# Performance work log

Measured on AMD Instinct MI355X. Metric: run time of the kernel, lower is better.

## Reference

```python
import jax, jax.numpy as jnp
import numpy as np

B, S, E, H, SN, LMAX = 128, 512, 768, 16, 100, 5
DH = E // H  # 48

def setup_inputs() -> dict:
    key = jax.random.key(0)
    ks = jax.random.split(key, 10)
    idx = jax.random.randint(ks[0], (B, LMAX), 0, S)
    lengths = jax.random.randint(ks[1], (B,), 1, LMAX + 1)
    valid = jnp.arange(LMAX)[None, :] < lengths[:, None]
    locations = jnp.where(valid, idx, -1)
    return {
        "last_hidden_state": jax.random.normal(ks[2], (B, S, E), jnp.float32),
        "sense_emb": jax.random.normal(ks[3], (B, SN, E), jnp.float32),
        "locations": locations,
        "in_proj_weight": jax.random.normal(ks[4], (3 * E, E), jnp.float32) * 0.02,
        "in_proj_bias": jax.random.normal(ks[5], (3 * E,), jnp.float32) * 0.02,
        "out_proj_weight": jax.random.normal(ks[6], (E, E), jnp.float32) * 0.02,
        "out_proj_bias": jax.random.normal(ks[7], (E,), jnp.float32) * 0.02,
        "linear_weight": jax.random.normal(ks[8], (SN, E), jnp.float32) * 0.02,
        "linear_bias": jax.random.normal(ks[9], (SN,), jnp.float32) * 0.02,
    }

def reference(last_hidden_state, sense_emb, locations, in_proj_weight, in_proj_bias,
              out_proj_weight, out_proj_bias, linear_weight, linear_bias):
    # Ragged gather + mean over the valid (non -1) token locations per row.
    mask = (locations != -1)                                   # [B, LMAX]
    safe = jnp.where(mask, locations, 0)                       # [B, LMAX]
    gathered = jnp.take_along_axis(last_hidden_state, safe[..., None], axis=1)  # [B,LMAX,E]
    cnt = mask.sum(axis=1, keepdims=True).astype(last_hidden_state.dtype)
    pun = (gathered * mask[..., None]).sum(axis=1) / cnt       # [B, E]

    # qkv: prepend pun-word embedding to the sense embeddings -> [B, SN+1, E]
    qkv = jnp.concatenate([pun[:, None, :], sense_emb], axis=1)

    # nn.MultiheadAttention with batch_first=False: axis0 = seq (L=B), axis1 = batch (N=SN+1).
    proj = qkv @ in_proj_weight.T + in_proj_bias               # [L, N, 3E]
    q, k, v = jnp.split(proj, 3, axis=-1)
    L, N = qkv.shape[0], qkv.shape[1]
    q = q.reshape(L, N, H, DH) * (DH ** -0.5)
    k = k.reshape(L, N, H, DH)
    v = v.reshape(L, N, H, DH)
    scores = jnp.einsum('lnhd,mnhd->nhlm', q, k)               # [N,H,L,L]
    attn = jax.nn.softmax(scores, axis=-1)
    ctx = jnp.einsum('nhlm,mnhd->lnhd', attn, v).reshape(L, N, E)
    attn_out = ctx @ out_proj_weight.T + out_proj_bias         # [L, N, E]

    res = attn_out[:, 0, :]                                    # [B, E] (batch slot 0)
    res = res @ linear_weight.T + linear_bias                  # [B, SN]
    return res
```

## Files before the change

kernel.cpp:

```cpp
#include <hip/hip_runtime.h>

#define SEQ 512
#define EMB 768
#define K3E 2304
#define DHD 48

__global__ __launch_bounds__(256) void k1_gemm1(
    const float* __restrict__ lhs, const int* __restrict__ loc,
    const float* __restrict__ Bw, const float* __restrict__ bias,
    float* __restrict__ C)
{
  __shared__ float lds[7168];
  const int t  = threadIdx.x;
  const int w  = t >> 6, l = t & 63;
  const int bm = blockIdx.y * 16, bn = blockIdx.x * 32;
  const int tx = l & 7, ty = l >> 3;
  const int gm = l & 15, gq = l >> 4;
  const int bl = l & 31, bh = l >> 5;
  const int kbase = w * 192;
  const int AW = w * 1792, BW = AW + 640;

  int locs[5]; int cnt = 0;
#pragma unroll
  for (int j = 0; j < 5; j++) {
    int v = loc[(bm + gm) * 5 + j];
    locs[j] = v; if (v >= 0) cnt++;
  }
  const float ginv = 1.0f / (float)cnt;
  const float* lrow = lhs + (size_t)(bm + gm) * SEQ * EMB;
  const float* brow = Bw + (size_t)(bn + bl) * EMB;

  float4 aF, bF0, bF1;

#define K1_LOAD(s) {                                                         \
    int k0 = kbase + (s) * 16;                                               \
    float sx=0.f, sy=0.f, sz=0.f, sw=0.f;                                    \
    _Pragma("unroll")                                                        \
    for (int j = 0; j < 5; j++) {                                            \
      int v = locs[j] >= 0 ? locs[j] : 0;                                    \
      float4 wv = *(const float4*)&lrow[(size_t)v * EMB + k0 + gq * 4];      \
      if (locs[j] >= 0) { sx+=wv.x; sy+=wv.y; sz+=wv.z; sw+=wv.w; }          \
    }                                                                        \
    aF = make_float4(sx*ginv, sy*ginv, sz*ginv, sw*ginv);                    \
    bF0 = *(const float4*)&brow[k0 + bh * 8 + 0];                            \
    bF1 = *(const float4*)&brow[k0 + bh * 8 + 4]; }

#define K1_WRITE(b) {                                                        \
    int Ab = AW + (b) * 320;                                                 \
    lds[Ab + (gq*4+0)*20 + gm] = aF.x;                                       \
    lds[Ab + (gq*4+1)*20 + gm] = aF.y;                                       \
    lds[Ab + (gq*4+2)*20 + gm] = aF.z;                                       \
    lds[Ab + (gq*4+3)*20 + gm] = aF.w;                                       \
    int Bb = BW + (b) * 576;                                                 \
    lds[Bb + (bh*8+0)*36 + bl] = bF0.x; lds[Bb + (bh*8+1)*36 + bl] = bF0.y;  \
    lds[Bb + (bh*8+2)*36 + bl] = bF0.z; lds[Bb + (bh*8+3)*36 + bl] = bF0.w;  \
    lds[Bb + (bh*8+4)*36 + bl] = bF1.x; lds[Bb + (bh*8+5)*36 + bl] = bF1.y;  \
    lds[Bb + (bh*8+6)*36 + bl] = bF1.z; lds[Bb + (bh*8+7)*36 + bl] = bF1.w; }

  float acc[2][4] = {};
  K1_LOAD(0); K1_WRITE(0);
  for (int s = 0; s < 12; s++) {
    int b = s & 1;
    if (s < 11) K1_LOAD(s + 1);
    int Ab = AW + b * 320, Bb = BW + b * 576;
#pragma unroll
    for (int kk = 0; kk < 16; kk++) {
      float2 a  = *(float2*)&lds[Ab + kk * 20 + ty * 2];
      float4 bb = *(float4*)&lds[Bb + kk * 36 + tx * 4];
      acc[0][0] += a.x*bb.x; acc[0][1] += a.x*bb.y; acc[0][2] += a.x*bb.z; acc[0][3] += a.x*bb.w;
      acc[1][0] += a.y*bb.x; acc[1][1] += a.y*bb.y; acc[1][2] += a.y*bb.z; acc[1][3] += a.y*bb.w;
    }
    if (s < 11) K1_WRITE(b ^ 1);
  }
#undef K1_LOAD
#undef K1_WRITE

#pragma unroll
  for (int i = 0; i < 2; i++)
    *(float4*)&lds[AW + (ty*2 + i) * 32 + tx * 4] =
        make_float4(acc[i][0], acc[i][1], acc[i][2], acc[i][3]);
  __syncthreads();
  int o = t * 2;
  int m = o >> 5, n = o & 31;
  float2 s0 = *(float2*)&lds[0*1792 + o];
  float2 s1 = *(float2*)&lds[1*1792 + o];
  float2 s2 = *(float2*)&lds[2*1792 + o];
  float2 s3 = *(float2*)&lds[3*1792 + o];
  float2 bb2 = *(const float2*)&bias[bn + n];
  float2 r = make_float2(s0.x+s1.x+s2.x+s3.x+bb2.x, s0.y+s1.y+s2.y+s3.y+bb2.y);
  *(float2*)&C[(size_t)(bm + m) * K3E + bn + n] = r;
}

__global__ __launch_bounds__(256) void k2_attn_wcomb(
    const float* __restrict__ proj, float* __restrict__ ctx,
    const float* __restrict__ wlin, const float* __restrict__ wout,
    float* __restrict__ wcomb)
{
  __shared__ float lds[13312];
  const int t = threadIdx.x;

  if (blockIdx.x < 128) {
    float* ks = lds;
    float* vs = lds + 6656;
    int h  = blockIdx.x >> 3;
    int l0 = (blockIdx.x & 7) * 16;

    for (int i = t; i < 128 * 12; i += 256) {
      int m  = i / 12;
      int dd = (i - m * 12) * 4;
      float4 kv = *(const float4*)&proj[(size_t)m * K3E + EMB     + h * DHD + dd];
      float4 vv = *(const float4*)&proj[(size_t)m * K3E + 2 * EMB + h * DHD + dd];
      *(float4*)&ks[m * 52 + dd] = kv;
      *(float4*)&vs[m * 52 + dd] = vv;
    }

    int l  = t >> 4;
    int g  = t & 15;
    int lg = l0 + l;
    const float scale = 0.14433756729740643f;
    float q[48];
#pragma unroll
    for (int jj = 0; jj < 12; jj++) {
      float4 qv = *(const float4*)&proj[(size_t)lg * K3E + h * DHD + jj * 4];
      q[jj*4+0] = qv.x * scale; q[jj*4+1] = qv.y * scale;
      q[jj*4+2] = qv.z * scale; q[jj*4+3] = qv.w * scale;
    }
    __syncthreads();

    float sv[8];
    float smax = -1e30f;
#pragma unroll
    for (int jm = 0; jm < 8; jm++) {
      int m = g + jm * 16;
      float s = 0.0f;
#pragma unroll
      for (int dq = 0; dq < 12; dq++) {
        float4 kv = *(const float4*)&ks[m * 52 + dq * 4];
        s += q[dq*4+0]*kv.x + q[dq*4+1]*kv.y + q[dq*4+2]*kv.z + q[dq*4+3]*kv.w;
      }
      sv[jm] = s;
      smax = fmaxf(smax, s);
    }
#pragma unroll
    for (int off = 1; off < 16; off <<= 1) smax = fmaxf(smax, __shfl_xor(smax, off));
    float ssum = 0.0f;
#pragma unroll
    for (int jm = 0; jm < 8; jm++) { float e = __expf(sv[jm] - smax); sv[jm] = e; ssum += e; }
#pragma unroll
    for (int off = 1; off < 16; off <<= 1) ssum += __shfl_xor(ssum, off);
    float inv = 1.0f / ssum;
#pragma unroll
    for (int jm = 0; jm < 8; jm++) sv[jm] *= inv;

    float acc[48] = {};
#pragma unroll
    for (int jm = 0; jm < 8; jm++) {
      int m = g + jm * 16;
      float p = sv[jm];
#pragma unroll
      for (int dq = 0; dq < 12; dq++) {
        float4 vv = *(const float4*)&vs[m * 52 + dq * 4];
        acc[dq*4+0] += p*vv.x; acc[dq*4+1] += p*vv.y;
        acc[dq*4+2] += p*vv.z; acc[dq*4+3] += p*vv.w;
      }
    }

    {
      float buf[24];
      if (g & 8) {
#pragma unroll
        for (int d = 0; d < 24; d++) buf[d] = acc[d];
      } else {
#pragma unroll
        for (int d = 0; d < 24; d++) buf[d] = acc[d + 24];
      }
#pragma unroll
      for (int d = 0; d < 24; d++) buf[d] = __shfl_xor(buf[d], 8);
      if (g & 8) {
#pragma unroll
        for (int d = 0; d < 24; d++) acc[d] = acc[d + 24] + buf[d];
      } else {
#pragma unroll
        for (int d = 0; d < 24; d++) acc[d] = acc[d] + buf[d];
      }
    }
    {
      float buf[12];
      if (g & 4) {
#pragma unroll
        for (int d = 0; d < 12; d++) buf[d] = acc[d];
      } else {
#pragma unroll
        for (int d = 0; d < 12; d++) buf[d] = acc[d + 12];
      }
#pragma unroll
      for (int d = 0; d < 12; d++) buf[d] = __shfl_xor(buf[d], 4);
      if (g & 4) {
#pragma unroll
        for (int d = 0; d < 12; d++) acc[d] = acc[d + 12] + buf[d];
      } else {
#pragma unroll
        for (int d = 0; d < 12; d++) acc[d] = acc[d] + buf[d];
      }
    }
    {
      float buf[6];
      if (g & 2) {
#pragma unroll
        for (int d = 0; d < 6; d++) buf[d] = acc[d];
      } else {
#pragma unroll
        for (int d = 0; d < 6; d++) buf[d] = acc[d + 6];
      }
#pragma unroll
      for (int d = 0; d < 6; d++) buf[d] = __shfl_xor(buf[d], 2);
      if (g & 2) {
#pragma unroll
        for (int d = 0; d < 6; d++) acc[d] = acc[d + 6] + buf[d];
      } else {
#pragma unroll
        for (int d = 0; d < 6; d++) acc[d] = acc[d] + buf[d];
      }
    }
    {
      float buf[3];
      if (g & 1) {
#pragma unroll
        for (int d = 0; d < 3; d++) buf[d] = acc[d];
      } else {
#pragma unroll
        for (int d = 0; d < 3; d++) buf[d] = acc[d + 3];
      }
#pragma unroll
      for (int d = 0; d < 3; d++) buf[d] = __shfl_xor(buf[d], 1);
      if (g & 1) {
#pragma unroll
        for (int d = 0; d < 3; d++) acc[d] = acc[d + 3] + buf[d];
      } else {
#pragma unroll
        for (int d = 0; d < 3; d++) acc[d] = acc[d] + buf[d];
      }
    }
#pragma unroll
    for (int j = 0; j < 3; j++) {
      ctx[(size_t)lg * EMB + h * DHD + g * 3 + j] = acc[j];
    }
  } else {
    const int c  = blockIdx.x - 128;
    const int bm = (c / 24) * 16;
    const int bn = (c % 24) * 32;
    const int w  = t >> 6, l = t & 63;
    const int tx = l & 7, ty = l >> 3;
    const int am = l & 15, aq = l >> 4;
    const int wi = l >> 2;
    const int j4 = (l & 3) * 8;
    const int kbase = w * 192;
    const int AW = w * 1792, BW = AW + 640;

    int arow_i = bm + am; if (arow_i > 99) arow_i = 99;
    const float* arow = wlin + (size_t)arow_i * EMB;

    float4 aF, bF0, bF1;

#define W_LOAD(s) {                                                          \
    int k0 = kbase + (s) * 16;                                               \
    aF  = *(const float4*)&arow[k0 + aq * 4];                                \
    const float* wr = wout + (size_t)(k0 + wi) * EMB + bn + j4;              \
    bF0 = *(const float4*)&wr[0];                                            \
    bF1 = *(const float4*)&wr[4]; }

#define W_WRITE(b) {                                                         \
    int Ab = AW + (b) * 320;                                                 \
    lds[Ab + (aq*4+0)*20 + am] = aF.x;                                       \
    lds[Ab + (aq*4+1)*20 + am] = aF.y;                                       \
    lds[Ab + (aq*4+2)*20 + am] = aF.z;                                       \
    lds[Ab + (aq*4+3)*20 + am] = aF.w;                                       \
    int Bb = BW + (b) * 576;                                                 \
    *(float4*)&lds[Bb + wi*36 + j4]     = bF0;                               \
    *(float4*)&lds[Bb + wi*36 + j4 + 4] = bF1; }

    float acc[2][4] = {};
    W_LOAD(0); W_WRITE(0);
    for (int s = 0; s < 12; s++) {
      int b = s & 1;
      if (s < 11) W_LOAD(s + 1);
      int Ab = AW + b * 320, Bb = BW + b * 576;
#pragma unroll
      for (int kk = 0; kk < 16; kk++) {
        float2 a  = *(float2*)&lds[Ab + kk * 20 + ty * 2];
        float4 bb = *(float4*)&lds[Bb + kk * 36 + tx * 4];
        acc[0][0] += a.x*bb.x; acc[0][1] += a.x*bb.y; acc[0][2] += a.x*bb.z; acc[0][3] += a.x*bb.w;
        acc[1][0] += a.y*bb.x; acc[1][1] += a.y*bb.y; acc[1][2] += a.y*bb.z; acc[1][3] += a.y*bb.w;
      }
      if (s < 11) W_WRITE(b ^ 1);
    }
#undef W_LOAD
#undef W_WRITE

#pragma unroll
    for (int i = 0; i < 2; i++)
      *(float4*)&lds[AW + (ty*2 + i) * 32 + tx * 4] =
          make_float4(acc[i][0], acc[i][1], acc[i][2], acc[i][3]);
    __syncthreads();
    int o = t * 2;
    int m = o >> 5, n = o & 31;
    if (bm + m < 100) {
      float2 s0 = *(float2*)&lds[0*1792 + o];
      float2 s1 = *(float2*)&lds[1*1792 + o];
      float2 s2 = *(float2*)&lds[2*1792 + o];
      float2 s3 = *(float2*)&lds[3*1792 + o];
      float2 r = make_float2(s0.x+s1.x+s2.x+s3.x, s0.y+s1.y+s2.y+s3.y);
      *(float2*)&wcomb[(size_t)(bm + m) * EMB + bn + n] = r;
    }
  }
}

__global__ __launch_bounds__(256) void k3_final(
    const float* __restrict__ A, const float* __restrict__ Bw,
    const float* __restrict__ wlin, const float* __restrict__ bout,
    const float* __restrict__ blin, float* __restrict__ C)
{
  __shared__ float lds[7200];
  const int t  = threadIdx.x;
  const int w  = t >> 6, l = t & 63;
  const int bm = blockIdx.y * 16, bn = blockIdx.x * 32;
  const int tx = l & 7, ty = l >> 3;
  const int am = l & 15, aq = l >> 4;
  const int bl = l & 31, bh = l >> 5;
  const int kbase = w * 192;
  const int AW = w * 1792, BW = AW + 640;

  {
    int col = bn + (t >> 3);
    int ks  = (t & 7) * 96;
    float p = 0.f;
    if (col < 100) {
      const float* wr = wlin + (size_t)col * EMB + ks;
#pragma unroll
      for (int j = 0; j < 24; j++) {
        float4 wv = *(const float4*)&wr[j * 4];
        float4 bv = *(const float4*)&bout[ks + j * 4];
        p += wv.x*bv.x + wv.y*bv.y + wv.z*bv.z + wv.w*bv.w;
      }
    }
    p += __shfl_xor(p, 1); p += __shfl_xor(p, 2); p += __shfl_xor(p, 4);
    if ((t & 7) == 0) lds[7168 + (t >> 3)] = p + (col < 100 ? blin[col] : 0.f);
  }

  const float* arow = A + (size_t)(bm + am) * EMB;
  int brow_i = bn + bl; if (brow_i > 99) brow_i = 99;
  const float* brow = Bw + (size_t)brow_i * EMB;

  float4 aF, bF0, bF1;

#define F_LOAD(s) {                                                          \
    int k0 = kbase + (s) * 16;                                               \
    aF  = *(const float4*)&arow[k0 + aq * 4];                                \
    bF0 = *(const float4*)&brow[k0 + bh * 8 + 0];                            \
    bF1 = *(const float4*)&brow[k0 + bh * 8 + 4]; }

#define F_WRITE(b) {                                                         \
    int Ab = AW + (b) * 320;                                                 \
    lds[Ab + (aq*4+0)*20 + am] = aF.x;                                       \
    lds[Ab + (aq*4+1)*20 + am] = aF.y;                                       \
    lds[Ab + (aq*4+2)*20 + am] = aF.z;                                       \
    lds[Ab + (aq*4+3)*20 + am] = aF.w;                                       \
    int Bb = BW + (b) * 576;                                                 \
    lds[Bb + (bh*8+0)*36 + bl] = bF0.x; lds[Bb + (bh*8+1)*36 + bl] = bF0.y;  \
    lds[Bb + (bh*8+2)*36 + bl] = bF0.z; lds[Bb + (bh*8+3)*36 + bl] = bF0.w;  \
    lds[Bb + (bh*8+4)*36 + bl] = bF1.x; lds[Bb + (bh*8+5)*36 + bl] = bF1.y;  \
    lds[Bb + (bh*8+6)*36 + bl] = bF1.z; lds[Bb + (bh*8+7)*36 + bl] = bF1.w; }

  float acc[2][4] = {};
  F_LOAD(0); F_WRITE(0);
  for (int s = 0; s < 12; s++) {
    int b = s & 1;
    if (s < 11) F_LOAD(s + 1);
    int Ab = AW + b * 320, Bb = BW + b * 576;
#pragma unroll
    for (int kk = 0; kk < 16; kk++) {
      float2 a  = *(float2*)&lds[Ab + kk * 20 + ty * 2];
      float4 bb = *(float4*)&lds[Bb + kk * 36 + tx * 4];
      acc[0][0] += a.x*bb.x; acc[0][1] += a.x*bb.y; acc[0][2] += a.x*bb.z; acc[0][3] += a.x*bb.w;
      acc[1][0] += a.y*bb.x; acc[1][1] += a.y*bb.y; acc[1][2] += a.y*bb.z; acc[1][3] += a.y*bb.w;
    }
    if (s < 11) F_WRITE(b ^ 1);
  }
#undef F_LOAD
#undef F_WRITE

#pragma unroll
  for (int i = 0; i < 2; i++)
    *(float4*)&lds[AW + (ty*2 + i) * 32 + tx * 4] =
        make_float4(acc[i][0], acc[i][1], acc[i][2], acc[i][3]);
  __syncthreads();
  int o = t * 2;
  int m = o >> 5, n = o & 31;
#pragma unroll
  for (int j = 0; j < 2; j++) {
    int col = bn + n + j;
    if (col < 100) {
      float v = lds[0*1792 + o + j] + lds[1*1792 + o + j] +
                lds[2*1792 + o + j] + lds[3*1792 + o + j] + lds[7168 + n + j];
      C[(size_t)(bm + m) * 100 + col] = v;
    }
  }
}

extern "C" void kernel_launch(void* const* d_in, const int* in_sizes, int n_in,
                              void* d_out, int out_size, void* d_ws, size_t ws_size,
                              hipStream_t stream) {
  const float* lhs   = (const float*)d_in[0];
  const int*   loc   = (const int*)  d_in[2];
  const float* w_in  = (const float*)d_in[3];
  const float* b_in  = (const float*)d_in[4];
  const float* w_out = (const float*)d_in[5];
  const float* b_out = (const float*)d_in[6];
  const float* w_lin = (const float*)d_in[7];
  const float* b_lin = (const float*)d_in[8];
  float* out = (float*)d_out;

  char* ws = (char*)d_ws;
  float* proj  = (float*)(ws);
  float* ctx   = (float*)(ws + 1179648);
  float* wcomb = (float*)(ws + 1179648 + 393216);

  k1_gemm1<<<dim3(72, 8), 256, 0, stream>>>(lhs, loc, w_in, b_in, proj);
  k2_attn_wcomb<<<296, 256, 0, stream>>>(proj, ctx, w_lin, w_out, wcomb);
  k3_final<<<dim3(4, 8), 256, 0, stream>>>(ctx, wcomb, w_lin, b_out, b_lin, out);
}
```

Baseline: 51.70 us.

## Split pun gather into own kernel, move wcomb GEMM into first GEMM launch, widen split-K

The ragged gather-mean moves out of the QKV GEMM into a separate small kernel, so the GEMM no longer re-gathers hidden-state rows for every N tile. The Wout·Wlin combination GEMM moves from the attention launch into the QKV GEMM launch, so attention runs alone. The GEMMs now use 512-thread blocks with 8-way split-K instead of 4-way. This shortens the serial K loop and raises parallelism, at the cost of one extra launch, a pun round trip through global memory, and an 8-way LDS reduction.

Result: faster. 45.93 us (-11.2%).

```diff
diff --git a/kernel.cpp b/kernel.cpp
--- a/kernel.cpp
+++ b/kernel.cpp
@@ -5,47 +5,349 @@
 #define K3E 2304
 #define DHD 48
 
-__global__ __launch_bounds__(256) void k1_gemm1(
+__global__ __launch_bounds__(256) void k0_pun(
     const float* __restrict__ lhs, const int* __restrict__ loc,
-    const float* __restrict__ Bw, const float* __restrict__ bias,
-    float* __restrict__ C)
+    float* __restrict__ pun)
 {
-  __shared__ float lds[7168];
-  const int t  = threadIdx.x;
-  const int w  = t >> 6, l = t & 63;
+  int id = blockIdx.x * 256 + threadIdx.x;
+  int row = id / 192;
+  int ch  = id - row * 192;
+  int cnt = 0;
+  float4 s = make_float4(0.f, 0.f, 0.f, 0.f);
+#pragma unroll
+  for (int j = 0; j < 5; j++) {
+    int v = loc[row * 5 + j];
+    if (v >= 0) {
+      float4 wv = *(const float4*)&lhs[((size_t)row * SEQ + v) * EMB + ch * 4];
+      s.x += wv.x; s.y += wv.y; s.z += wv.z; s.w += wv.w;
+      cnt++;
+    }
+  }
+  float inv = 1.0f / (float)cnt;
+  *(float4*)&pun[(size_t)row * EMB + ch * 4] =
+      make_float4(s.x * inv, s.y * inv, s.z * inv, s.w * inv);
+}
+
+__global__ __launch_bounds__(512, 4) void k1_gemm_wcomb(
+    const float* __restrict__ pun, const float* __restrict__ Bw,
+    const float* __restrict__ bias, float* __restrict__ C,
+    const float* __restrict__ wlin, const float* __restrict__ wout,
+    float* __restrict__ wcomb)
+{
+  __shared__ float lds[14336];
+  const int t = threadIdx.x;
+  const int w = t >> 6, l = t & 63;
+  const int tx = l & 7, ty = l >> 3;
+  const int gm = l & 15, gq = l >> 4;
+  const int kbase = w * 96;
+  const int AW = w * 1792, BW = AW + 640;
+
+  float4 aF, bF0, bF1;
+  float acc[2][4] = {};
+
+#define STAGE_A(b) {                                                         \
+    int Ab = AW + (b) * 320;                                                 \
+    lds[Ab + (gq*4+0)*20 + gm] = aF.x;                                       \
+    lds[Ab + (gq*4+1)*20 + gm] = aF.y;                                       \
+    lds[Ab + (gq*4+2)*20 + gm] = aF.z;                                       \
+    lds[Ab + (gq*4+3)*20 + gm] = aF.w; }
+
+#define INNER(b) {                                                           \
+    int Ab = AW + (b) * 320, Bb = BW + (b) * 576;                            \
+    _Pragma("unroll")                                                        \
+    for (int kk = 0; kk < 16; kk++) {                                        \
+      float2 a  = *(float2*)&lds[Ab + kk * 20 + ty * 2];                     \
+      float4 bb = *(float4*)&lds[Bb + kk * 36 + tx * 4];                     \
+      acc[0][0] += a.x*bb.x; acc[0][1] += a.x*bb.y;                          \
+      acc[0][2] += a.x*bb.z; acc[0][3] += a.x*bb.w;                          \
+      acc[1][0] += a.y*bb.x; acc[1][1] += a.y*bb.y;                          \
+      acc[1][2] += a.y*bb.z; acc[1][3] += a.y*bb.w;                          \
+    } }
+
+  if (blockIdx.x < 576) {
+    const int c  = blockIdx.x;
+    const int bm = (c / 72) * 16, bn = (c % 72) * 32;
+    const int bl = l & 31, bh = l >> 5;
+    const float* arow = pun + (size_t)(bm + gm) * EMB;
+    const float* brow = Bw + (size_t)(bn + bl) * EMB;
+
+#define G_LOAD(s) {                                                          \
+    int k0 = kbase + (s) * 16;                                               \
+    aF  = *(const float4*)&arow[k0 + gq * 4];                                \
+    bF0 = *(const float4*)&brow[k0 + bh * 8 + 0];                            \
+    bF1 = *(const float4*)&brow[k0 + bh * 8 + 4]; }
+
+#define G_WRITE(b) {                                                         \
+    STAGE_A(b)                                                               \
+    int Bb = BW + (b) * 576;                                                 \
+    lds[Bb + (bh*8+0)*36 + bl] = bF0.x; lds[Bb + (bh*8+1)*36 + bl] = bF0.y;  \
+    lds[Bb + (bh*8+2)*36 + bl] = bF0.z; lds[Bb + (bh*8+3)*36 + bl] = bF0.w;  \
+    lds[Bb + (bh*8+4)*36 + bl] = bF1.x; lds[Bb + (bh*8+5)*36 + bl] = bF1.y;  \
+    lds[Bb + (bh*8+6)*36 + bl] = bF1.z; lds[Bb + (bh*8+7)*36 + bl] = bF1.w; }
+
+    G_LOAD(0); G_WRITE(0);
+    for (int s = 0; s < 6; s++) {
+      int b = s & 1;
+      if (s < 5) G_LOAD(s + 1);
+      INNER(b);
+      if (s < 5) G_WRITE(b ^ 1);
+    }
+#undef G_LOAD
+#undef G_WRITE
+
+#pragma unroll
+    for (int i = 0; i < 2; i++)
+      *(float4*)&lds[AW + (ty*2 + i) * 32 + tx * 4] =
+          make_float4(acc[i][0], acc[i][1], acc[i][2], acc[i][3]);
+    __syncthreads();
+    int m = t >> 5, n = t & 31;
+    float v = lds[0*1792 + t] + lds[1*1792 + t] + lds[2*1792 + t] + lds[3*1792 + t]
+            + lds[4*1792 + t] + lds[5*1792 + t] + lds[6*1792 + t] + lds[7*1792 + t]
+            + bias[bn + n];
+    C[(size_t)(bm + m) * K3E + bn + n] = v;
+  } else {
+    const int cc = blockIdx.x - 576;
+    const int bm = (cc / 24) * 16, bn = (cc % 24) * 32;
+    const int wi = l >> 2;
+    const int j4 = (l & 3) * 8;
+    int arow_i = bm + gm; if (arow_i > 99) arow_i = 99;
+    const float* arow = wlin + (size_t)arow_i * EMB;
+
+#define W_LOAD(s) {                                                          \
+    int k0 = kbase + (s) * 16;                                               \
+    aF  = *(const float4*)&arow[k0 + gq * 4];                                \
+    const float* wr = wout + (size_t)(k0 + wi) * EMB + bn + j4;              \
+    bF0 = *(const float4*)&wr[0];                                            \
+    bF1 = *(const float4*)&wr[4]; }
+
+#define W_WRITE(b) {                                                         \
+    STAGE_A(b)                                                               \
+    int Bb = BW + (b) * 576;                                                 \
+    *(float4*)&lds[Bb + wi*36 + j4]     = bF0;                               \
+    *(float4*)&lds[Bb + wi*36 + j4 + 4] = bF1; }
+
+    W_LOAD(0); W_WRITE(0);
+    for (int s = 0; s < 6; s++) {
+      int b = s & 1;
+      if (s < 5) W_LOAD(s + 1);
+      INNER(b);
+      if (s < 5) W_WRITE(b ^ 1);
+    }
+#undef W_LOAD
+#undef W_WRITE
+
+#pragma unroll
+    for (int i = 0; i < 2; i++)
+      *(float4*)&lds[AW + (ty*2 + i) * 32 + tx * 4] =
+          make_float4(acc[i][0], acc[i][1], acc[i][2], acc[i][3]);
+    __syncthreads();
+    int m = t >> 5, n = t & 31;
+    if (bm + m < 100) {
+      float v = lds[0*1792 + t] + lds[1*1792 + t] + lds[2*1792 + t] + lds[3*1792 + t]
+              + lds[4*1792 + t] + lds[5*1792 + t] + lds[6*1792 + t] + lds[7*1792 + t];
+      wcomb[(size_t)(bm + m) * EMB + bn + n] = v;
+    }
+  }
+#undef STAGE_A
+#undef INNER
+}
+
+__global__ __launch_bounds__(256) void k2_attn(
+    const float* __restrict__ proj, float* __restrict__ ctx)
+{
+  __shared__ float ks[128][52];
+  __shared__ float vs[128][52];
+  int h  = blockIdx.x >> 3;
+  int l0 = (blockIdx.x & 7) * 16;
+  int t  = threadIdx.x;
+
+  for (int i = t; i < 128 * 12; i += 256) {
+    int m  = i / 12;
+    int dd = (i - m * 12) * 4;
+    float4 kv = *(const float4*)&proj[(size_t)m * K3E + EMB     + h * DHD + dd];
+    float4 vv = *(const float4*)&proj[(size_t)m * K3E + 2 * EMB + h * DHD + dd];
+    *(float4*)&ks[m][dd] = kv;
+    *(float4*)&vs[m][dd] = vv;
+  }
+
+  int l  = t >> 4;
+  int g  = t & 15;
+  int lg = l0 + l;
+  const float scale = 0.14433756729740643f;
+  float q[48];
+#pragma unroll
+  for (int jj = 0; jj < 12; jj++) {
+    float4 qv = *(const float4*)&proj[(size_t)lg * K3E + h * DHD + jj * 4];
+    q[jj*4+0] = qv.x * scale; q[jj*4+1] = qv.y * scale;
+    q[jj*4+2] = qv.z * scale; q[jj*4+3] = qv.w * scale;
+  }
+  __syncthreads();
+
+  float sv[8];
+  float smax = -1e30f;
+#pragma unroll
+  for (int jm = 0; jm < 8; jm++) {
+    int m = g + jm * 16;
+    float s = 0.0f;
+#pragma unroll
+    for (int dq = 0; dq < 12; dq++) {
+      float4 kv = *(const float4*)&ks[m][dq * 4];
+      s += q[dq*4+0]*kv.x + q[dq*4+1]*kv.y + q[dq*4+2]*kv.z + q[dq*4+3]*kv.w;
+    }
+    sv[jm] = s;
+    smax = fmaxf(smax, s);
+  }
+#pragma unroll
+  for (int off = 1; off < 16; off <<= 1) smax = fmaxf(smax, __shfl_xor(smax, off));
+  float ssum = 0.0f;
+#pragma unroll
+  for (int jm = 0; jm < 8; jm++) { float e = __expf(sv[jm] - smax); sv[jm] = e; ssum += e; }
+#pragma unroll
+  for (int off = 1; off < 16; off <<= 1) ssum += __shfl_xor(ssum, off);
+  float inv = 1.0f / ssum;
+#pragma unroll
+  for (int jm = 0; jm < 8; jm++) sv[jm] *= inv;
+
+  float acc[48] = {};
+#pragma unroll
+  for (int jm = 0; jm < 8; jm++) {
+    int m = g + jm * 16;
+    float p = sv[jm];
+#pragma unroll
+    for (int dq = 0; dq < 12; dq++) {
+      float4 vv = *(const float4*)&vs[m][dq * 4];
+      acc[dq*4+0] += p*vv.x; acc[dq*4+1] += p*vv.y;
+      acc[dq*4+2] += p*vv.z; acc[dq*4+3] += p*vv.w;
+    }
+  }
+
+  {
+    float buf[24];
+    if (g & 8) {
+#pragma unroll
+      for (int d = 0; d < 24; d++) buf[d] = acc[d];
+    } else {
+#pragma unroll
+      for (int d = 0; d < 24; d++) buf[d] = acc[d + 24];
+    }
+#pragma unroll
+    for (int d = 0; d < 24; d++) buf[d] = __shfl_xor(buf[d], 8);
+    if (g & 8) {
+#pragma unroll
+      for (int d = 0; d < 24; d++) acc[d] = acc[d + 24] + buf[d];
+    } else {
+#pragma unroll
+      for (int d = 0; d < 24; d++) acc[d] = acc[d] + buf[d];
+    }
+  }
+  {
+    float buf[12];
+    if (g & 4) {
+#pragma unroll
+      for (int d = 0; d < 12; d++) buf[d] = acc[d];
+    } else {
+#pragma unroll
+      for (int d = 0; d < 12; d++) buf[d] = acc[d + 12];
+    }
+#pragma unroll
+    for (int d = 0; d < 12; d++) buf[d] = __shfl_xor(buf[d], 4);
+    if (g & 4) {
+#pragma unroll
+      for (int d = 0; d < 12; d++) acc[d] = acc[d + 12] + buf[d];
+    } else {
+#pragma unroll
+      for (int d = 0; d < 12; d++) acc[d] = acc[d] + buf[d];
+    }
+  }
+  {
+    float buf[6];
+    if (g & 2) {
+#pragma unroll
+      for (int d = 0; d < 6; d++) buf[d] = acc[d];
+    } else {
+#pragma unroll
+      for (int d = 0; d < 6; d++) buf[d] = acc[d + 6];
+    }
+#pragma unroll
+    for (int d = 0; d < 6; d++) buf[d] = __shfl_xor(buf[d], 2);
+    if (g & 2) {
+#pragma unroll
+      for (int d = 0; d < 6; d++) acc[d] = acc[d + 6] + buf[d];
+    } else {
+#pragma unroll
+      for (int d = 0; d < 6; d++) acc[d] = acc[d] + buf[d];
+    }
+  }
+  {
+    float buf[3];
+    if (g & 1) {
+#pragma unroll
+      for (int d = 0; d < 3; d++) buf[d] = acc[d];
+    } else {
+#pragma unroll
+      for (int d = 0; d < 3; d++) buf[d] = acc[d + 3];
+    }
+#pragma unroll
+    for (int d = 0; d < 3; d++) buf[d] = __shfl_xor(buf[d], 1);
+    if (g & 1) {
+#pragma unroll
+      for (int d = 0; d < 3; d++) acc[d] = acc[d + 3] + buf[d];
+    } else {
+#pragma unroll
+      for (int d = 0; d < 3; d++) acc[d] = acc[d] + buf[d];
+    }
+  }
+#pragma unroll
+  for (int j = 0; j < 3; j++) {
+    ctx[(size_t)lg * EMB + h * DHD + g * 3 + j] = acc[j];
+  }
+}
+
+__global__ __launch_bounds__(512, 4) void k3_final(
+    const float* __restrict__ A, const float* __restrict__ Bw,
+    const float* __restrict__ wlin, const float* __restrict__ bout,
+    const float* __restrict__ blin, float* __restrict__ C)
+{
+  __shared__ float lds[14368];
+  const int t = threadIdx.x;
+  const int w = t >> 6, l = t & 63;
   const int bm = blockIdx.y * 16, bn = blockIdx.x * 32;
   const int tx = l & 7, ty = l >> 3;
   const int gm = l & 15, gq = l >> 4;
   const int bl = l & 31, bh = l >> 5;
-  const int kbase = w * 192;
+  const int kbase = w * 96;
   const int AW = w * 1792, BW = AW + 640;
 
-  int locs[5]; int cnt = 0;
-#pragma unroll
-  for (int j = 0; j < 5; j++) {
-    int v = loc[(bm + gm) * 5 + j];
-    locs[j] = v; if (v >= 0) cnt++;
-  }
-  const float ginv = 1.0f / (float)cnt;
-  const float* lrow = lhs + (size_t)(bm + gm) * SEQ * EMB;
-  const float* brow = Bw + (size_t)(bn + bl) * EMB;
+  if (t < 256) {
+    int col = bn + (t >> 3);
+    int ks  = (t & 7) * 96;
+    float p = 0.f;
+    if (col < 100) {
+      const float* wr = wlin + (size_t)col * EMB + ks;
+#pragma unroll
+      for (int j = 0; j < 24; j++) {
+        float4 wv = *(const float4*)&wr[j * 4];
+        float4 bv = *(const float4*)&bout[ks + j * 4];
+        p += wv.x*bv.x + wv.y*bv.y + wv.z*bv.z + wv.w*bv.w;
+      }
+    }
+    p += __shfl_xor(p, 1); p += __shfl_xor(p, 2); p += __shfl_xor(p, 4);
+    if ((t & 7) == 0) lds[14336 + (t >> 3)] = p + (col < 100 ? blin[col] : 0.f);
+  }
+
+  const float* arow = A + (size_t)(bm + gm) * EMB;
+  int brow_i = bn + bl; if (brow_i > 99) brow_i = 99;
+  const float* brow = Bw + (size_t)brow_i * EMB;
 
   float4 aF, bF0, bF1;
 
-#define K1_LOAD(s) {                                                         \
+#define F_LOAD(s) {                                                          \
     int k0 = kbase + (s) * 16;                                               \
-    float sx=0.f, sy=0.f, sz=0.f, sw=0.f;                                    \
-    _Pragma("unroll")                                                        \
-    for (int j = 0; j < 5; j++) {                                            \
-      int v = locs[j] >= 0 ? locs[j] : 0;                                    \
-      float4 wv = *(const float4*)&lrow[(size_t)v * EMB + k0 + gq * 4];      \
-      if (locs[j] >= 0) { sx+=wv.x; sy+=wv.y; sz+=wv.z; sw+=wv.w; }          \
-    }                                                                        \
-    aF = make_float4(sx*ginv, sy*ginv, sz*ginv, sw*ginv);                    \
+    aF  = *(const float4*)&arow[k0 + gq * 4];                                \
     bF0 = *(const float4*)&brow[k0 + bh * 8 + 0];                            \
     bF1 = *(const float4*)&brow[k0 + bh * 8 + 4]; }
 
-#define K1_WRITE(b) {                                                        \
+#define F_WRITE(b) {                                                         \
     int Ab = AW + (b) * 320;                                                 \
     lds[Ab + (gq*4+0)*20 + gm] = aF.x;                                       \
     lds[Ab + (gq*4+1)*20 + gm] = aF.y;                                       \
@@ -58,10 +360,10 @@
     lds[Bb + (bh*8+6)*36 + bl] = bF1.z; lds[Bb + (bh*8+7)*36 + bl] = bF1.w; }
 
   float acc[2][4] = {};
-  K1_LOAD(0); K1_WRITE(0);
-  for (int s = 0; s < 12; s++) {
+  F_LOAD(0); F_WRITE(0);
+  for (int s = 0; s < 6; s++) {
     int b = s & 1;
-    if (s < 11) K1_LOAD(s + 1);
+    if (s < 5) F_LOAD(s + 1);
     int Ab = AW + b * 320, Bb = BW + b * 576;
 #pragma unroll
     for (int kk = 0; kk < 16; kk++) {
@@ -70,340 +372,23 @@
       acc[0][0] += a.x*bb.x; acc[0][1] += a.x*bb.y; acc[0][2] += a.x*bb.z; acc[0][3] += a.x*bb.w;
       acc[1][0] += a.y*bb.x; acc[1][1] += a.y*bb.y; acc[1][2] += a.y*bb.z; acc[1][3] += a.y*bb.w;
     }
-    if (s < 11) K1_WRITE(b ^ 1);
-  }
-#undef K1_LOAD
-#undef K1_WRITE
+    if (s < 5) F_WRITE(b ^ 1);
+  }
+#undef F_LOAD
+#undef F_WRITE
 
 #pragma unroll
   for (int i = 0; i < 2; i++)
     *(float4*)&lds[AW + (ty*2 + i) * 32 + tx * 4] =
         make_float4(acc[i][0], acc[i][1], acc[i][2], acc[i][3]);
   __syncthreads();
-  int o = t * 2;
-  int m = o >> 5, n = o & 31;
-  float2 s0 = *(float2*)&lds[0*1792 + o];
-  float2 s1 = *(float2*)&lds[1*1792 + o];
-  float2 s2 = *(float2*)&lds[2*1792 + o];
-  float2 s3 = *(float2*)&lds[3*1792 + o];
-  float2 bb2 = *(const float2*)&bias[bn + n];
-  float2 r = make_float2(s0.x+s1.x+s2.x+s3.x+bb2.x, s0.y+s1.y+s2.y+s3.y+bb2.y);
-  *(float2*)&C[(size_t)(bm + m) * K3E + bn + n] = r;
-}
-
-__global__ __launch_bounds__(256) void k2_attn_wcomb(
-    const float* __restrict__ proj, float* __restrict__ ctx,
-    const float* __restrict__ wlin, const float* __restrict__ wout,
-    float* __restrict__ wcomb)
-{
-  __shared__ float lds[13312];
-  const int t = threadIdx.x;
-
-  if (blockIdx.x < 128) {
-    float* ks = lds;
-    float* vs = lds + 6656;
-    int h  = blockIdx.x >> 3;
-    int l0 = (blockIdx.x & 7) * 16;
-
-    for (int i = t; i < 128 * 12; i += 256) {
-      int m  = i / 12;
-      int dd = (i - m * 12) * 4;
-      float4 kv = *(const float4*)&proj[(size_t)m * K3E + EMB     + h * DHD + dd];
-      float4 vv = *(const float4*)&proj[(size_t)m * K3E + 2 * EMB + h * DHD + dd];
-      *(float4*)&ks[m * 52 + dd] = kv;
-      *(float4*)&vs[m * 52 + dd] = vv;
-    }
-
-    int l  = t >> 4;
-    int g  = t & 15;
-    int lg = l0 + l;
-    const float scale = 0.14433756729740643f;
-    float q[48];
-#pragma unroll
-    for (int jj = 0; jj < 12; jj++) {
-      float4 qv = *(const float4*)&proj[(size_t)lg * K3E + h * DHD + jj * 4];
-      q[jj*4+0] = qv.x * scale; q[jj*4+1] = qv.y * scale;
-      q[jj*4+2] = qv.z * scale; q[jj*4+3] = qv.w * scale;
-    }
-    __syncthreads();
-
-    float sv[8];
-    float smax = -1e30f;
-#pragma unroll
-    for (int jm = 0; jm < 8; jm++) {
-      int m = g + jm * 16;
-      float s = 0.0f;
-#pragma unroll
-      for (int dq = 0; dq < 12; dq++) {
-        float4 kv = *(const float4*)&ks[m * 52 + dq * 4];
-        s += q[dq*4+0]*kv.x + q[dq*4+1]*kv.y + q[dq*4+2]*kv.z + q[dq*4+3]*kv.w;
-      }
-      sv[jm] = s;
-      smax = fmaxf(smax, s);
-    }
-#pragma unroll
-    for (int off = 1; off < 16; off <<= 1) smax = fmaxf(smax, __shfl_xor(smax, off));
-    float ssum = 0.0f;
-#pragma unroll
-    for (int jm = 0; jm < 8; jm++) { float e = __expf(sv[jm] - smax); sv[jm] = e; ssum += e; }
-#pragma unroll
-    for (int off = 1; off < 16; off <<= 1) ssum += __shfl_xor(ssum, off);
-    float inv = 1.0f / ssum;
-#pragma unroll
-    for (int jm = 0; jm < 8; jm++) sv[jm] *= inv;
-
-    float acc[48] = {};
-#pragma unroll
-    for (int jm = 0; jm < 8; jm++) {
-      int m = g + jm * 16;
-      float p = sv[jm];
-#pragma unroll
-      for (int dq = 0; dq < 12; dq++) {
-        float4 vv = *(const float4*)&vs[m * 52 + dq * 4];
-        acc[dq*4+0] += p*vv.x; acc[dq*4+1] += p*vv.y;
-        acc[dq*4+2] += p*vv.z; acc[dq*4+3] += p*vv.w;
-      }
-    }
-
-    {
-      float buf[24];
-      if (g & 8) {
-#pragma unroll
-        for (int d = 0; d < 24; d++) buf[d] = acc[d];
-      } else {
-#pragma unroll
-        for (int d = 0; d < 24; d++) buf[d] = acc[d + 24];
-      }
-#pragma unroll
-      for (int d = 0; d < 24; d++) buf[d] = __shfl_xor(buf[d], 8);
-      if (g & 8) {
-#pragma unroll
-        for (int d = 0; d < 24; d++) acc[d] = acc[d + 24] + buf[d];
-      } else {
-#pragma unroll
-        for (int d = 0; d < 24; d++) acc[d] = acc[d] + buf[d];
-      }
-    }
-    {
-      float buf[12];
-      if (g & 4) {
-#pragma unroll
-        for (int d = 0; d < 12; d++) buf[d] = acc[d];
-      } else {
-#pragma unroll
-        for (int d = 0; d < 12; d++) buf[d] = acc[d + 12];
-      }
-#pragma unroll
-      for (int d = 0; d < 12; d++) buf[d] = __shfl_xor(buf[d], 4);
-      if (g & 4) {
-#pragma unroll
-        for (int d = 0; d < 12; d++) acc[d] = acc[d + 12] + buf[d];
-      } else {
-#pragma unroll
-        for (int d = 0; d < 12; d++) acc[d] = acc[d] + buf[d];
-      }
-    }
-    {
-      float buf[6];
-      if (g & 2) {
-#pragma unroll
-        for (int d = 0; d < 6; d++) buf[d] = acc[d];
-      } else {
-#pragma unroll
-        for (int d = 0; d < 6; d++) buf[d] = acc[d + 6];
-      }
-#pragma unroll
-      for (int d = 0; d < 6; d++) buf[d] = __shfl_xor(buf[d], 2);
-      if (g & 2) {
-#pragma unroll
-        for (int d = 0; d < 6; d++) acc[d] = acc[d + 6] + buf[d];
-      } else {
-#pragma unroll
-        for (int d = 0; d < 6; d++) acc[d] = acc[d] + buf[d];
-      }
-    }
-    {
-      float buf[3];
-      if (g & 1) {
-#pragma unroll
-        for (int d = 0; d < 3; d++) buf[d] = acc[d];
-      } else {
-#pragma unroll
-        for (int d = 0; d < 3; d++) buf[d] = acc[d + 3];
-      }
-#pragma unroll
-      for (int d = 0; d < 3; d++) buf[d] = __shfl_xor(buf[d], 1);
-      if (g & 1) {
-#pragma unroll
-        for (int d = 0; d < 3; d++) acc[d] = acc[d + 3] + buf[d];
-      } else {
-#pragma unroll
-        for (int d = 0; d < 3; d++) acc[d] = acc[d] + buf[d];
-      }
-    }
-#pragma unroll
-    for (int j = 0; j < 3; j++) {
-      ctx[(size_t)lg * EMB + h * DHD + g * 3 + j] = acc[j];
-    }
-  } else {
-    const int c  = blockIdx.x - 128;
-    const int bm = (c / 24) * 16;
-    const int bn = (c % 24) * 32;
-    const int w  = t >> 6, l = t & 63;
-    const int tx = l & 7, ty = l >> 3;
-    const int am = l & 15, aq = l >> 4;
-    const int wi = l >> 2;
-    const int j4 = (l & 3) * 8;
-    const int kbase = w * 192;
-    const int AW = w * 1792, BW = AW + 640;
-
-    int arow_i = bm + am; if (arow_i > 99) arow_i = 99;
-    const float* arow = wlin + (size_t)arow_i * EMB;
-
-    float4 aF, bF0, bF1;
-
-#define W_LOAD(s) {                                                          \
-    int k0 = kbase + (s) * 16;                                               \
-    aF  = *(const float4*)&arow[k0 + aq * 4];                                \
-    const float* wr = wout + (size_t)(k0 + wi) * EMB + bn + j4;              \
-    bF0 = *(const float4*)&wr[0];                                            \
-    bF1 = *(const float4*)&wr[4]; }
-
-#define W_WRITE(b) {                                                         \
-    int Ab = AW + (b) * 320;                                                 \
-    lds[Ab + (aq*4+0)*20 + am] = aF.x;                                       \
-    lds[Ab + (aq*4+1)*20 + am] = aF.y;                                       \
-    lds[Ab + (aq*4+2)*20 + am] = aF.z;                                       \
-    lds[Ab + (aq*4+3)*20 + am] = aF.w;                                       \
-    int Bb = BW + (b) * 576;                                                 \
-    *(float4*)&lds[Bb + wi*36 + j4]     = bF0;                               \
-    *(float4*)&lds[Bb + wi*36 + j4 + 4] = bF1; }
-
-    float acc[2][4] = {};
-    W_LOAD(0); W_WRITE(0);
-    for (int s = 0; s < 12; s++) {
-      int b = s & 1;
-      if (s < 11) W_LOAD(s + 1);
-      int Ab = AW + b * 320, Bb = BW + b * 576;
-#pragma unroll
-      for (int kk = 0; kk < 16; kk++) {
-        float2 a  = *(float2*)&lds[Ab + kk * 20 + ty * 2];
-        float4 bb = *(float4*)&lds[Bb + kk * 36 + tx * 4];
-        acc[0][0] += a.x*bb.x; acc[0][1] += a.x*bb.y; acc[0][2] += a.x*bb.z; acc[0][3] += a.x*bb.w;
-        acc[1][0] += a.y*bb.x; acc[1][1] += a.y*bb.y; acc[1][2] += a.y*bb.z; acc[1][3] += a.y*bb.w;
-      }
-      if (s < 11) W_WRITE(b ^ 1);
-    }
-#undef W_LOAD
-#undef W_WRITE
-
-#pragma unroll
-    for (int i = 0; i < 2; i++)
-      *(float4*)&lds[AW + (ty*2 + i) * 32 + tx * 4] =
-          make_float4(acc[i][0], acc[i][1], acc[i][2], acc[i][3]);
-    __syncthreads();
-    int o = t * 2;
-    int m = o >> 5, n = o & 31;
-    if (bm + m < 100) {
-      float2 s0 = *(float2*)&lds[0*1792 + o];
-      float2 s1 = *(float2*)&lds[1*1792 + o];
-      float2 s2 = *(float2*)&lds[2*1792 + o];
-      float2 s3 = *(float2*)&lds[3*1792 + o];
-      float2 r = make_float2(s0.x+s1.x+s2.x+s3.x, s0.y+s1.y+s2.y+s3.y);
-      *(float2*)&wcomb[(size_t)(bm + m) * EMB + bn + n] = r;
-    }
-  }
-}
-
-__global__ __launch_bounds__(256) void k3_final(
-    const float* __restrict__ A, const float* __restrict__ Bw,
-    const float* __restrict__ wlin, const float* __restrict__ bout,
-    const float* __restrict__ blin, float* __restrict__ C)
-{
-  __shared__ float lds[7200];
-  const int t  = threadIdx.x;
-  const int w  = t >> 6, l = t & 63;
-  const int bm = blockIdx.y * 16, bn = blockIdx.x * 32;
-  const int tx = l & 7, ty = l >> 3;
-  const int am = l & 15, aq = l >> 4;
-  const int bl = l & 31, bh = l >> 5;
-  const int kbase = w * 192;
-  const int AW = w * 1792, BW = AW + 640;
-
-  {
-    int col = bn + (t >> 3);
-    int ks  = (t & 7) * 96;
-    float p = 0.f;
-    if (col < 100) {
-      const float* wr = wlin + (size_t)col * EMB + ks;
-#pragma unroll
-      for (int j = 0; j < 24; j++) {
-        float4 wv = *(const float4*)&wr[j * 4];
-        float4 bv = *(const float4*)&bout[ks + j * 4];
-        p += wv.x*bv.x + wv.y*bv.y + wv.z*bv.z + wv.w*bv.w;
-      }
-    }
-    p += __shfl_xor(p, 1); p += __shfl_xor(p, 2); p += __shfl_xor(p, 4);
-    if ((t & 7) == 0) lds[7168 + (t >> 3)] = p + (col < 100 ? blin[col] : 0.f);
-  }
-
-  const float* arow = A + (size_t)(bm + am) * EMB;
-  int brow_i = bn + bl; if (brow_i > 99) brow_i = 99;
-  const float* brow = Bw + (size_t)brow_i * EMB;
-
-  float4 aF, bF0, bF1;
-
-#define F_LOAD(s) {                                                          \
-    int k0 = kbase + (s) * 16;                                               \
-    aF  = *(const float4*)&arow[k0 + aq * 4];                                \
-    bF0 = *(const float4*)&brow[k0 + bh * 8 + 0];                            \
-    bF1 = *(const float4*)&brow[k0 + bh * 8 + 4]; }
-
-#define F_WRITE(b) {                                                         \
-    int Ab = AW + (b) * 320;                                                 \
-    lds[Ab + (aq*4+0)*20 + am] = aF.x;                                       \
-    lds[Ab + (aq*4+1)*20 + am] = aF.y;                                       \
-    lds[Ab + (aq*4+2)*20 + am] = aF.z;                                       \
-    lds[Ab + (aq*4+3)*20 + am] = aF.w;                                       \
-    int Bb = BW + (b) * 576;                                                 \
-    lds[Bb + (bh*8+0)*36 + bl] = bF0.x; lds[Bb + (bh*8+1)*36 + bl] = bF0.y;  \
-    lds[Bb + (bh*8+2)*36 + bl] = bF0.z; lds[Bb + (bh*8+3)*36 + bl] = bF0.w;  \
-    lds[Bb + (bh*8+4)*36 + bl] = bF1.x; lds[Bb + (bh*8+5)*36 + bl] = bF1.y;  \
-    lds[Bb + (bh*8+6)*36 + bl] = bF1.z; lds[Bb + (bh*8+7)*36 + bl] = bF1.w; }
-
-  float acc[2][4] = {};
-  F_LOAD(0); F_WRITE(0);
-  for (int s = 0; s < 12; s++) {
-    int b = s & 1;
-    if (s < 11) F_LOAD(s + 1);
-    int Ab = AW + b * 320, Bb = BW + b * 576;
-#pragma unroll
-    for (int kk = 0; kk < 16; kk++) {
-      float2 a  = *(float2*)&lds[Ab + kk * 20 + ty * 2];
-      float4 bb = *(float4*)&lds[Bb + kk * 36 + tx * 4];
-      acc[0][0] += a.x*bb.x; acc[0][1] += a.x*bb.y; acc[0][2] += a.x*bb.z; acc[0][3] += a.x*bb.w;
-      acc[1][0] += a.y*bb.x; acc[1][1] += a.y*bb.y; acc[1][2] += a.y*bb.z; acc[1][3] += a.y*bb.w;
-    }
-    if (s < 11) F_WRITE(b ^ 1);
-  }
-#undef F_LOAD
-#undef F_WRITE
-
-#pragma unroll
-  for (int i = 0; i < 2; i++)
-    *(float4*)&lds[AW + (ty*2 + i) * 32 + tx * 4] =
-        make_float4(acc[i][0], acc[i][1], acc[i][2], acc[i][3]);
-  __syncthreads();
-  int o = t * 2;
-  int m = o >> 5, n = o & 31;
-#pragma unroll
-  for (int j = 0; j < 2; j++) {
-    int col = bn + n + j;
-    if (col < 100) {
-      float v = lds[0*1792 + o + j] + lds[1*1792 + o + j] +
-                lds[2*1792 + o + j] + lds[3*1792 + o + j] + lds[7168 + n + j];
-      C[(size_t)(bm + m) * 100 + col] = v;
-    }
+  int m = t >> 5, n = t & 31;
+  int col = bn + n;
+  if (col < 100) {
+    float v = lds[0*1792 + t] + lds[1*1792 + t] + lds[2*1792 + t] + lds[3*1792 + t]
+            + lds[4*1792 + t] + lds[5*1792 + t] + lds[6*1792 + t] + lds[7*1792 + t]
+            + lds[14336 + n];
+    C[(size_t)(bm + m) * 100 + col] = v;
   }
 }
 
@@ -421,11 +406,14 @@
   float* out = (float*)d_out;
 
   char* ws = (char*)d_ws;
-  float* proj  = (float*)(ws);
-  float* ctx   = (float*)(ws + 1179648);
-  float* wcomb = (float*)(ws + 1179648 + 393216);
-
-  k1_gemm1<<<dim3(72, 8), 256, 0, stream>>>(lhs, loc, w_in, b_in, proj);
-  k2_attn_wcomb<<<296, 256, 0, stream>>>(proj, ctx, w_lin, w_out, wcomb);
-  k3_final<<<dim3(4, 8), 256, 0, stream>>>(ctx, wcomb, w_lin, b_out, b_lin, out);
+  float* pun   = (float*)(ws);
+  float* proj  = (float*)(ws + 393216);
+  float* ctx   = (float*)(ws + 393216 + 1179648);
+  float* wcomb = (float*)(ws + 393216 + 1179648 + 393216);
+
+  k0_pun<<<96, 256, 0, stream>>>(lhs, loc, pun);
+  k1_gemm_wcomb<<<744, 512, 0, stream>>>(pun, w_in, b_in, proj,
+                                         w_lin, w_out, wcomb);
+  k2_attn<<<128, 256, 0, stream>>>(proj, ctx);
+  k3_final<<<dim3(4, 8), 512, 0, stream>>>(ctx, wcomb, w_lin, b_out, b_lin, out);
 }
```
